# Kernel optimization log

Measured on AMD Instinct MI355X. Metric: run time of the kernel, lower is better.

Reference implementation:

```python
import jax, jax.numpy as jnp
import numpy as np

IN_FEATURES = 2048
OUT_FEATURES = 2048
BATCH = 4096


def setup_inputs() -> dict:
    key = jax.random.key(0)
    k1, k2, k3, k4 = jax.random.split(key, 4)
    bound = 1.0 / (IN_FEATURES ** 0.5)
    x_re = jax.random.normal(k1, (BATCH, IN_FEATURES), dtype=jnp.float32)
    x_im = jax.random.normal(k2, (BATCH, IN_FEATURES), dtype=jnp.float32)
    # filters: (out_features, in_features), re/im each uniform(-bound, bound)
    w_re = jax.random.uniform(k3, (OUT_FEATURES, IN_FEATURES), dtype=jnp.float32, minval=-bound, maxval=bound)
    w_im = jax.random.uniform(k4, (OUT_FEATURES, IN_FEATURES), dtype=jnp.float32, minval=-bound, maxval=bound)
    return {"x_re": x_re, "x_im": x_im, "w_re": w_re, "w_im": w_im}


def reference(x_re, x_im, w_re, w_im):
    # Complex linear: (x_re + i x_im) @ (w_re + i w_im)^T, expressed as 4 real GEMMs.
    # Equivalent to torch: (inputs.unsqueeze(1) * filters).sum(-1) with complex64.
    out_re = jnp.einsum('bi,oi->bo', x_re, w_re) - jnp.einsum('bi,oi->bo', x_im, w_im)
    out_im = jnp.einsum('bi,oi->bo', x_re, w_im) + jnp.einsum('bi,oi->bo', x_im, w_re)
    # stack re/im -> (2, batch, out) to keep a single real-dtype output
    return jnp.stack([out_re, out_im], axis=0)
```

## Files before the change

### kernel.cpp

```cpp
#include <hip/hip_runtime.h>

typedef __bf16 bf16_t;
typedef __bf16 bf16x8 __attribute__((ext_vector_type(8)));
typedef __bf16 bf16x4 __attribute__((ext_vector_type(4)));
typedef float f32x4 __attribute__((ext_vector_type(4)));

#define M_DIM 4096
#define N_DIM 4096
#define K_DIM 4096
#define OUTF 2048
#define INF 2048
#define LDK 4096
#define NT 64

__global__ __launch_bounds__(256) void pack_ab(
    const float* __restrict__ xre, const float* __restrict__ xim,
    const float* __restrict__ wre, const float* __restrict__ wim,
    bf16_t* __restrict__ Abf, bf16_t* __restrict__ Bbf)
{
  size_t gid = (size_t)blockIdx.x * 256 + threadIdx.x;
  size_t e8  = gid * 8;
  const size_t MAT = (size_t)4096 * 4096;
  bool isB = e8 >= MAT;
  size_t e = isB ? (e8 - MAT) : e8;
  int row = (int)(e >> 12);
  int k   = (int)(e & 4095);

  const float* src;
  float s = 1.0f;
  if (!isB) {
    src = (k < INF) ? (xre + (size_t)row * INF + k)
                    : (xim + (size_t)row * INF + (k - INF));
  } else {
    if (row < OUTF) {
      if (k < INF) { src = wre + (size_t)row * INF + k; }
      else         { src = wim + (size_t)row * INF + (k - INF); s = -1.0f; }
    } else {
      int o = row - OUTF;
      src = (k < INF) ? (wim + (size_t)o * INF + k)
                      : (wre + (size_t)o * INF + (k - INF));
    }
  }
  const float4* p = reinterpret_cast<const float4*>(src);
  float4 f0 = p[0];
  float4 f1 = p[1];
  bf16x8 v;
  v[0] = (bf16_t)(f0.x * s); v[1] = (bf16_t)(f0.y * s);
  v[2] = (bf16_t)(f0.z * s); v[3] = (bf16_t)(f0.w * s);
  v[4] = (bf16_t)(f1.x * s); v[5] = (bf16_t)(f1.y * s);
  v[6] = (bf16_t)(f1.z * s); v[7] = (bf16_t)(f1.w * s);
  bf16_t* dst = (isB ? Bbf : Abf) + e;
  *reinterpret_cast<bf16x8*>(dst) = v;
}

__device__ __forceinline__ void gld_lds16(const void* g, void* l) {
  __builtin_amdgcn_global_load_lds(
      (const __attribute__((address_space(1))) void*)g,
      (__attribute__((address_space(3))) void*)l,
      16, 0, 0);
}


template<int QM, int QN>
__device__ __forceinline__ void mfma_quad(f32x4 (&acc)[8][4],
                                          const bf16x8 (&aF)[4][2],
                                          const bf16x8 (&bF)[2][2]) {
  __builtin_amdgcn_s_setprio(1);
#pragma unroll
  for (int m = 0; m < 4; ++m)
#pragma unroll
    for (int n = 0; n < 2; ++n) {
      f32x4 v = acc[QM * 4 + m][QN * 2 + n];
      v = __builtin_amdgcn_mfma_f32_16x16x32_bf16(aF[m][0], bF[n][0], v, 0, 0, 0);
      v = __builtin_amdgcn_mfma_f32_16x16x32_bf16(aF[m][1], bF[n][1], v, 0, 0, 0);
      acc[QM * 4 + m][QN * 2 + n] = v;
    }
  __builtin_amdgcn_s_setprio(0);
}

__global__ __launch_bounds__(512, 2) void gemm256(
    const bf16_t* __restrict__ A, const bf16_t* __restrict__ B,
    float* __restrict__ out)
{
  __shared__ alignas(16) bf16_t lds[2 * 32768];
  char* Lb = (char*)lds;

  const int tid  = threadIdx.x;
  const int lane = tid & 63;
  const int wid  = tid >> 6;
  const int wm   = wid >> 2;
  const int wn   = wid & 3;
  const int lr   = lane & 15;
  const int kg   = (lane >> 4) * 16;
  const int xm   = ((lr & 3) << 4) | (((lr >> 2) & 1) << 6);

  int bid = blockIdx.x;
  int swz = (bid & 7) * 32 + (bid >> 3);
  const int bm = swz >> 4;
  const int bn = swz & 15;

  int rS[2], kS[2];
#pragma unroll
  for (int j = 0; j < 2; ++j) {
    int P   = j * 8192 + tid * 16;
    int row = P >> 7;
    int p   = P & 127;
    int L   = p ^ ((row & 3) << 4) ^ (((row >> 2) & 1) << 6);
    rS[j] = row;
    kS[j] = L >> 1;
  }
  const bf16_t* As0 = A + (size_t)(bm * 256 + rS[0]) * LDK + kS[0];
  const bf16_t* As1 = A + (size_t)(bm * 256 + rS[1]) * LDK + kS[1];
  const bf16_t* Bs0 = B + (size_t)(bn * 256 + rS[0]) * LDK + kS[0];
  const bf16_t* Bs1 = B + (size_t)(bn * 256 + rS[1]) * LDK + kS[1];
  const int dst16 = tid * 16;

#define STAGE_A(t, h, c) do {                                                  \
    gld_lds16(As0 + (size_t)(h) * 128 * LDK + (t) * 64,                        \
              Lb + (c) * 65536 + (h) * 16384 + dst16);                         \
    gld_lds16(As1 + (size_t)(h) * 128 * LDK + (t) * 64,                        \
              Lb + (c) * 65536 + (h) * 16384 + 8192 + dst16);                  \
  } while (0)
#define STAGE_B(t, h, c) do {                                                  \
    gld_lds16(Bs0 + (size_t)(h) * 128 * LDK + (t) * 64,                        \
              Lb + (c) * 65536 + 32768 + (h) * 16384 + dst16);                 \
    gld_lds16(Bs1 + (size_t)(h) * 128 * LDK + (t) * 64,                        \
              Lb + (c) * 65536 + 32768 + (h) * 16384 + 8192 + dst16);          \
  } while (0)
#define RD_A(c, qm, m, ks)                                                     \
  (*(const bf16x8*)(Lb + (c) * 65536 + wm * 16384 +                            \
                    ((qm) * 64 + (m) * 16 + lr) * 128 +                        \
                    ((((ks) * 64) | kg) ^ xm)))
#define RD_B(c, qn, n, ks)                                                     \
  (*(const bf16x8*)(Lb + (c) * 65536 + 32768 + (wn >> 1) * 16384 +             \
                    ((wn & 1) * 64 + (qn) * 32 + (n) * 16 + lr) * 128 +        \
                    ((((ks) * 64) | kg) ^ xm)))
#define BAR()   __builtin_amdgcn_s_barrier()
#define SB()    __builtin_amdgcn_sched_barrier(0)

  f32x4 acc[8][4];
#pragma unroll
  for (int i = 0; i < 8; ++i)
#pragma unroll
    for (int j = 0; j < 4; ++j)
      acc[i][j] = (f32x4){0.f, 0.f, 0.f, 0.f};

  STAGE_A(0, 0, 0); STAGE_A(0, 1, 0);
  STAGE_B(0, 0, 0); STAGE_B(0, 1, 0);
  STAGE_A(1, 0, 1);
  asm volatile("s_waitcnt vmcnt(2)" ::: "memory");
  BAR();

  for (int t = 0; t < NT; ++t) {
    const int c = t & 1;
    bf16x8 a0[4][2], a1[4][2], b0[2][2], b1[2][2];

#pragma unroll
    for (int m = 0; m < 4; ++m) {
      a0[m][0] = RD_A(c, 0, m, 0);
      a0[m][1] = RD_A(c, 0, m, 1);
    }
#pragma unroll
    for (int n = 0; n < 2; ++n) {
      b0[n][0] = RD_B(c, 0, n, 0);
      b0[n][1] = RD_B(c, 0, n, 1);
    }
    SB();
#pragma unroll
    for (int n = 0; n < 2; ++n) {
      b1[n][0] = RD_B(c, 1, n, 0);
      b1[n][1] = RD_B(c, 1, n, 1);
    }
    SB();
    if (t + 1 < NT) STAGE_A(t + 1, 1, c ^ 1);
    asm volatile("s_waitcnt lgkmcnt(4)" ::: "memory");
    SB();
    mfma_quad<0, 0>(acc, a0, b0);
    BAR();

#pragma unroll
    for (int m = 0; m < 4; ++m) {
      a1[m][0] = RD_A(c, 1, m, 0);
      a1[m][1] = RD_A(c, 1, m, 1);
    }
    SB();
    if (t + 1 < NT) STAGE_B(t + 1, 0, c ^ 1);
    asm volatile("s_waitcnt lgkmcnt(8)" ::: "memory");
    SB();
    mfma_quad<0, 1>(acc, a0, b1);
    BAR();

    if (t + 1 < NT) STAGE_B(t + 1, 1, c ^ 1);
    asm volatile("s_waitcnt lgkmcnt(0)" ::: "memory");
    SB();
    mfma_quad<1, 1>(acc, a1, b1);
    BAR();

    if (t + 2 < NT) STAGE_A(t + 2, 0, c);
    mfma_quad<1, 0>(acc, a1, b0);
    if (t + 2 < NT) {
      asm volatile("s_waitcnt vmcnt(2)" ::: "memory");
    } else if (t + 1 < NT) {
      asm volatile("s_waitcnt vmcnt(0)" ::: "memory");
    }
    BAR();
  }

  const size_t imOff = (size_t)M_DIM * OUTF;
  const int fq = (lane >> 4) * 4;
  const bool isIm = (bn * 256) >= OUTF;
  float* obase = out + (isIm ? imOff : 0);
  const int colBase = bn * 256 - (isIm ? OUTF : 0) + wn * 64;
#pragma unroll
  for (int ar = 0; ar < 8; ++ar) {
    int gr = bm * 256 + wm * 128 + ar * 16 + fq;
#pragma unroll
    for (int cc = 0; cc < 4; ++cc) {
      int gc = colBase + cc * 16 + lr;
#pragma unroll
      for (int j = 0; j < 4; ++j)
        obase[(size_t)(gr + j) * OUTF + gc] = acc[ar][cc][j];
    }
  }
#undef STAGE_A
#undef STAGE_B
#undef RD_A
#undef RD_B
#undef BAR
#undef SB
}

__global__ __launch_bounds__(256) void gemm_fused(
    const float* __restrict__ xre, const float* __restrict__ xim,
    const float* __restrict__ wre, const float* __restrict__ wim,
    float* __restrict__ out)
{
  __shared__ alignas(16) bf16_t As[128 * 40];
  __shared__ alignas(16) bf16_t Bs[128 * 40];

  int tid = threadIdx.x;
  int bid = blockIdx.x;
  int swz = (bid & 7) * 128 + (bid >> 3);
  int bm = swz >> 5;
  int bn = swz & 31;

  int lane = tid & 63;
  int w    = tid >> 6;
  int wm   = (w >> 1) * 64;
  int wn   = (w & 1) * 64;
  int lr   = lane & 15;
  int lk   = (lane >> 4) * 8;

  f32x4 acc[4][4];
#pragma unroll
  for (int m = 0; m < 4; ++m)
#pragma unroll
    for (int n = 0; n < 4; ++n)
      acc[m][n] = (f32x4){0.f, 0.f, 0.f, 0.f};

  int srow = tid >> 3;
  int scol = (tid & 7) * 4;

  bool nIm  = (bn * 128) >= OUTF;
  int nbase = nIm ? (bn * 128 - OUTF) : (bn * 128);

  for (int kt = 0; kt < K_DIM / 32; ++kt) {
    int k0 = kt * 32;
    bool kHi = (k0 >= INF);
    int kk = kHi ? (k0 - INF) : k0;

    const float* Asrc = (kHi ? xim : xre) + (size_t)(bm * 128) * INF + kk;
    const float* Bsrc;
    float s = 1.0f;
    if (!nIm) { if (!kHi) { Bsrc = wre; } else { Bsrc = wim; s = -1.0f; } }
    else      { Bsrc = kHi ? wre : wim; }
    Bsrc += (size_t)nbase * INF + kk;

    float4 av[4], bv[4];
#pragma unroll
    for (int i = 0; i < 4; ++i) {
      av[i] = *reinterpret_cast<const float4*>(Asrc + (size_t)(srow + i * 32) * INF + scol);
      bv[i] = *reinterpret_cast<const float4*>(Bsrc + (size_t)(srow + i * 32) * INF + scol);
    }
    __syncthreads();
#pragma unroll
    for (int i = 0; i < 4; ++i) {
      bf16x4 a4, b4;
      a4[0] = (bf16_t)av[i].x; a4[1] = (bf16_t)av[i].y;
      a4[2] = (bf16_t)av[i].z; a4[3] = (bf16_t)av[i].w;
      b4[0] = (bf16_t)(bv[i].x * s); b4[1] = (bf16_t)(bv[i].y * s);
      b4[2] = (bf16_t)(bv[i].z * s); b4[3] = (bf16_t)(bv[i].w * s);
      *reinterpret_cast<bf16x4*>(&As[(srow + i * 32) * 40 + scol]) = a4;
      *reinterpret_cast<bf16x4*>(&Bs[(srow + i * 32) * 40 + scol]) = b4;
    }
    __syncthreads();

    bf16x8 a[4], b[4];
#pragma unroll
    for (int m = 0; m < 4; ++m)
      a[m] = *reinterpret_cast<const bf16x8*>(&As[(wm + m * 16 + lr) * 40 + lk]);
#pragma unroll
    for (int n = 0; n < 4; ++n)
      b[n] = *reinterpret_cast<const bf16x8*>(&Bs[(wn + n * 16 + lr) * 40 + lk]);
#pragma unroll
    for (int m = 0; m < 4; ++m)
#pragma unroll
      for (int n = 0; n < 4; ++n)
        acc[m][n] = __builtin_amdgcn_mfma_f32_16x16x32_bf16(a[m], b[n], acc[m][n], 0, 0, 0);
  }
  __syncthreads();

  const size_t imOff = (size_t)M_DIM * OUTF;
  int fq = (lane >> 4) * 4;
#pragma unroll
  for (int m = 0; m < 4; ++m) {
    int gr = bm * 128 + wm + m * 16 + fq;
#pragma unroll
    for (int n = 0; n < 4; ++n) {
      int gc = bn * 128 + wn + n * 16 + lr;
      float* dst = (gc < OUTF) ? (out + (size_t)gr * OUTF + gc)
                               : (out + imOff + (size_t)gr * OUTF + (gc - OUTF));
#pragma unroll
      for (int j = 0; j < 4; ++j)
        dst[(size_t)j * OUTF] = acc[m][n][j];
    }
  }
}

extern "C" void kernel_launch(void* const* d_in, const int* in_sizes, int n_in,
                              void* d_out, int out_size, void* d_ws, size_t ws_size,
                              hipStream_t stream) {
  const float* xre = (const float*)d_in[0];
  const float* xim = (const float*)d_in[1];
  const float* wre = (const float*)d_in[2];
  const float* wim = (const float*)d_in[3];
  float* out = (float*)d_out;

  const size_t need = (size_t)2 * 4096 * 4096 * sizeof(bf16_t);
  if (ws_size >= need) {
    bf16_t* Abf = (bf16_t*)d_ws;
    bf16_t* Bbf = Abf + (size_t)4096 * 4096;
    hipLaunchKernelGGL(pack_ab, dim3(16384), dim3(256), 0, stream,
                       xre, xim, wre, wim, Abf, Bbf);
    hipLaunchKernelGGL(gemm256, dim3(256), dim3(512), 0, stream,
                       Abf, Bbf, out);
  } else {
    hipLaunchKernelGGL(gemm_fused, dim3(1024), dim3(256), 0, stream,
                       xre, xim, wre, wim, out);
  }
}
```

Before: 145.6 us.

## Prefetch next tile's first LDS fragments during final MFMA quad and drop barriers

The first quadrant's A/B fragment reads from LDS for the next k-tile are hoisted into the end of the current iteration, issued right after the last MFMA quad, with a prologue read before the loop. Two intra-iteration barriers are removed and the global-to-LDS stage issues are moved ahead of the LDS reads. The aim is to hide LDS read latency behind MFMA work and cut synchronisation stalls. In exchange, a0/b0 stay live across iterations, which raises register pressure. The hand-written lgkmcnt wait counts now depend on the new issue order, so correctness and the barrier removal rely on those counts still matching.

```diff
diff --git a/kernel.cpp b/kernel.cpp
--- a/kernel.cpp
+++ b/kernel.cpp
@@ -137,6 +137,18 @@
                     ((((ks) * 64) | kg) ^ xm)))
 #define BAR()   __builtin_amdgcn_s_barrier()
 #define SB()    __builtin_amdgcn_sched_barrier(0)
+#define ISSUE_Q1(c) do {                                                       \
+    _Pragma("unroll")                                                          \
+    for (int m_ = 0; m_ < 4; ++m_) {                                           \
+      a0[m_][0] = RD_A(c, 0, m_, 0);                                           \
+      a0[m_][1] = RD_A(c, 0, m_, 1);                                           \
+    }                                                                          \
+    _Pragma("unroll")                                                          \
+    for (int n_ = 0; n_ < 2; ++n_) {                                           \
+      b0[n_][0] = RD_B(c, 0, n_, 0);                                           \
+      b0[n_][1] = RD_B(c, 0, n_, 1);                                           \
+    }                                                                          \
+  } while (0)
 
   f32x4 acc[8][4];
 #pragma unroll
@@ -144,51 +156,42 @@
 #pragma unroll
     for (int j = 0; j < 4; ++j)
       acc[i][j] = (f32x4){0.f, 0.f, 0.f, 0.f};
+
+  bf16x8 a0[4][2], b0[2][2];
 
   STAGE_A(0, 0, 0); STAGE_A(0, 1, 0);
   STAGE_B(0, 0, 0); STAGE_B(0, 1, 0);
   STAGE_A(1, 0, 1);
   asm volatile("s_waitcnt vmcnt(2)" ::: "memory");
   BAR();
+  ISSUE_Q1(0);
+  SB();
 
   for (int t = 0; t < NT; ++t) {
     const int c = t & 1;
-    bf16x8 a0[4][2], a1[4][2], b0[2][2], b1[2][2];
-
-#pragma unroll
-    for (int m = 0; m < 4; ++m) {
-      a0[m][0] = RD_A(c, 0, m, 0);
-      a0[m][1] = RD_A(c, 0, m, 1);
-    }
-#pragma unroll
-    for (int n = 0; n < 2; ++n) {
-      b0[n][0] = RD_B(c, 0, n, 0);
-      b0[n][1] = RD_B(c, 0, n, 1);
-    }
-    SB();
+    bf16x8 a1[4][2], b1[2][2];
+
+    if (t + 1 < NT) STAGE_A(t + 1, 1, c ^ 1);
 #pragma unroll
     for (int n = 0; n < 2; ++n) {
       b1[n][0] = RD_B(c, 1, n, 0);
       b1[n][1] = RD_B(c, 1, n, 1);
     }
     SB();
-    if (t + 1 < NT) STAGE_A(t + 1, 1, c ^ 1);
     asm volatile("s_waitcnt lgkmcnt(4)" ::: "memory");
     SB();
     mfma_quad<0, 0>(acc, a0, b0);
-    BAR();
-
+
+    if (t + 1 < NT) STAGE_B(t + 1, 0, c ^ 1);
 #pragma unroll
     for (int m = 0; m < 4; ++m) {
       a1[m][0] = RD_A(c, 1, m, 0);
       a1[m][1] = RD_A(c, 1, m, 1);
     }
     SB();
-    if (t + 1 < NT) STAGE_B(t + 1, 0, c ^ 1);
     asm volatile("s_waitcnt lgkmcnt(8)" ::: "memory");
     SB();
     mfma_quad<0, 1>(acc, a0, b1);
-    BAR();
 
     if (t + 1 < NT) STAGE_B(t + 1, 1, c ^ 1);
     asm volatile("s_waitcnt lgkmcnt(0)" ::: "memory");
@@ -197,13 +200,18 @@
     BAR();
 
     if (t + 2 < NT) STAGE_A(t + 2, 0, c);
-    mfma_quad<1, 0>(acc, a1, b0);
     if (t + 2 < NT) {
       asm volatile("s_waitcnt vmcnt(2)" ::: "memory");
     } else if (t + 1 < NT) {
       asm volatile("s_waitcnt vmcnt(0)" ::: "memory");
     }
     BAR();
+    mfma_quad<1, 0>(acc, a1, b0);
+    if (t + 1 < NT) {
+      SB();
+      ISSUE_Q1(c ^ 1);
+      SB();
+    }
   }
 
   const size_t imOff = (size_t)M_DIM * OUTF;
@@ -228,6 +236,7 @@
 #undef RD_B
 #undef BAR
 #undef SB
+#undef ISSUE_Q1
 }
 
 __global__ __launch_bounds__(256) void gemm_fused(
```

Measured after the change: 141.9 us, median of 2. 2.6% less time.

## Software-pipeline LDS fragment reads across iterations with deeper global prefetch

Applied to the files above, without the earlier changes.

Restructures the main GEMM loop so the a0/b0 register fragments for the next tile are read from LDS during the current iteration's later MFMA quads, and issues global-to-LDS staging for tile t+2 earlier, which keeps more loads in flight. The aim is to hide LDS read latency and global load latency behind MFMA work and to cut the number of stalls at barriers. In exchange it uses more live registers and relies on more delicate vmcnt/lgkmcnt bookkeeping, where a wrong count could cause a race.

```diff
diff --git a/kernel.cpp b/kernel.cpp
--- a/kernel.cpp
+++ b/kernel.cpp
@@ -145,64 +145,74 @@
     for (int j = 0; j < 4; ++j)
       acc[i][j] = (f32x4){0.f, 0.f, 0.f, 0.f};
 
+  bf16x8 a0[4][2], b0[2][2];
+
   STAGE_A(0, 0, 0); STAGE_A(0, 1, 0);
   STAGE_B(0, 0, 0); STAGE_B(0, 1, 0);
-  STAGE_A(1, 0, 1);
-  asm volatile("s_waitcnt vmcnt(2)" ::: "memory");
+  STAGE_A(1, 0, 1); STAGE_B(1, 0, 1); STAGE_A(1, 1, 1);
+  asm volatile("s_waitcnt vmcnt(6)" ::: "memory");
   BAR();
+#pragma unroll
+  for (int m = 0; m < 4; ++m) { a0[m][0] = RD_A(0, 0, m, 0); a0[m][1] = RD_A(0, 0, m, 1); }
+#pragma unroll
+  for (int n = 0; n < 2; ++n) { b0[n][0] = RD_B(0, 0, n, 0); b0[n][1] = RD_B(0, 0, n, 1); }
+  SB();
 
   for (int t = 0; t < NT; ++t) {
     const int c = t & 1;
-    bf16x8 a0[4][2], a1[4][2], b0[2][2], b1[2][2];
-
-#pragma unroll
-    for (int m = 0; m < 4; ++m) {
-      a0[m][0] = RD_A(c, 0, m, 0);
-      a0[m][1] = RD_A(c, 0, m, 1);
-    }
-#pragma unroll
-    for (int n = 0; n < 2; ++n) {
-      b0[n][0] = RD_B(c, 0, n, 0);
-      b0[n][1] = RD_B(c, 0, n, 1);
-    }
-    SB();
-#pragma unroll
-    for (int n = 0; n < 2; ++n) {
-      b1[n][0] = RD_B(c, 1, n, 0);
-      b1[n][1] = RD_B(c, 1, n, 1);
-    }
-    SB();
-    if (t + 1 < NT) STAGE_A(t + 1, 1, c ^ 1);
-    asm volatile("s_waitcnt lgkmcnt(4)" ::: "memory");
+    bf16x8 a1[4][2], b1[2][2];
+
+    if (t + 1 < NT) STAGE_B(t + 1, 1, c ^ 1);
+#pragma unroll
+    for (int n = 0; n < 2; ++n) { b1[n][0] = RD_B(c, 1, n, 0); b1[n][1] = RD_B(c, 1, n, 1); }
+    a1[0][0] = RD_A(c, 1, 0, 0); a1[0][1] = RD_A(c, 1, 0, 1);
+    SB(); BAR();
+    asm volatile("s_waitcnt lgkmcnt(6)" ::: "memory");
     SB();
     mfma_quad<0, 0>(acc, a0, b0);
-    BAR();
-
-#pragma unroll
-    for (int m = 0; m < 4; ++m) {
-      a1[m][0] = RD_A(c, 1, m, 0);
-      a1[m][1] = RD_A(c, 1, m, 1);
-    }
-    SB();
-    if (t + 1 < NT) STAGE_B(t + 1, 0, c ^ 1);
+
+    if (t + 2 < NT) STAGE_A(t + 2, 0, c);
+#pragma unroll
+    for (int m = 1; m < 4; ++m) { a1[m][0] = RD_A(c, 1, m, 0); a1[m][1] = RD_A(c, 1, m, 1); }
+    SB(); BAR();
     asm volatile("s_waitcnt lgkmcnt(8)" ::: "memory");
     SB();
     mfma_quad<0, 1>(acc, a0, b1);
-    BAR();
-
-    if (t + 1 < NT) STAGE_B(t + 1, 1, c ^ 1);
-    asm volatile("s_waitcnt lgkmcnt(0)" ::: "memory");
+    if (t + 1 < NT) {
+      if (t + 2 < NT) asm volatile("s_waitcnt vmcnt(4)" ::: "memory");
+      else            asm volatile("s_waitcnt vmcnt(2)" ::: "memory");
+      BAR();
+    }
+
+    if (t + 2 < NT) STAGE_B(t + 2, 0, c);
+    if (t + 1 < NT) {
+#pragma unroll
+      for (int m = 0; m < 3; ++m) {
+        a0[m][0] = RD_A(c ^ 1, 0, m, 0); a0[m][1] = RD_A(c ^ 1, 0, m, 1);
+      }
+      SB(); BAR();
+      asm volatile("s_waitcnt lgkmcnt(6)" ::: "memory");
+    } else {
+      SB(); BAR();
+      asm volatile("s_waitcnt lgkmcnt(0)" ::: "memory");
+    }
     SB();
     mfma_quad<1, 1>(acc, a1, b1);
-    BAR();
-
-    if (t + 2 < NT) STAGE_A(t + 2, 0, c);
+
+    if (t + 2 < NT) STAGE_A(t + 2, 1, c);
+    SB();
     mfma_quad<1, 0>(acc, a1, b0);
-    if (t + 2 < NT) {
-      asm volatile("s_waitcnt vmcnt(2)" ::: "memory");
-    } else if (t + 1 < NT) {
-      asm volatile("s_waitcnt vmcnt(0)" ::: "memory");
-    }
+    SB();
+    if (t + 1 < NT) {
+      a0[3][0] = RD_A(c ^ 1, 0, 3, 0); a0[3][1] = RD_A(c ^ 1, 0, 3, 1);
+#pragma unroll
+      for (int n = 0; n < 2; ++n) {
+        b0[n][0] = RD_B(c ^ 1, 0, n, 0); b0[n][1] = RD_B(c ^ 1, 0, n, 1);
+      }
+      SB();
+    }
+    if (t + 2 < NT)      asm volatile("s_waitcnt vmcnt(6)" ::: "memory");
+    else if (t + 1 < NT) asm volatile("s_waitcnt vmcnt(0)" ::: "memory");
     BAR();
   }
 
```

New measurement: 145.1 us. About the same (-0.4%).
